# Kernel optimization log

Hardware: AMD Instinct MI355X
Metric: run time of the kernel (lower is better)

## Reference

```python
import jax, jax.numpy as jnp
import numpy as np

INIT_MEAN = 0.3


def _loo_sum(x, idx, n_seg):
    # leave-one-out segment sum along edge axis; x: [B, E]
    tot = jnp.zeros((x.shape[0], n_seg), x.dtype).at[:, idx].add(x)
    return tot[:, idx] - x


def _check_node_process(x, chk_idx, n_checks):
    # 2*atanh( prod_{e' in check, e'!=e} tanh(x_e'/2) ) via log-magnitude + sign
    t = jnp.tanh(0.5 * x)
    abs_t = jnp.clip(jnp.abs(t), 1e-12, None)
    log_loo = _loo_sum(jnp.log(abs_t), chk_idx, n_checks)
    neg = (t < 0).astype(x.dtype)
    neg_loo = _loo_sum(neg, chk_idx, n_checks)
    sign = 1.0 - 2.0 * jnp.mod(neg_loo, 2.0)
    prod = jnp.clip(sign * jnp.exp(log_loo), -1.0 + 1e-7, 1.0 - 1e-7)
    return 2.0 * jnp.arctanh(prod)


def setup_inputs() -> dict:
    N, M, DV, DC, ITERS, B = 8192, 4096, 3, 6, 5, 1024
    E = N * DV
    rng = np.random.RandomState(0)
    # regular (3,6) Tanner graph: each variable has 3 edges, each check 6
    var_idx = np.repeat(np.arange(N, dtype=np.int32), DV)
    chk_idx = rng.permutation(np.repeat(np.arange(M, dtype=np.int32), DC)).astype(np.int32)
    key = jax.random.key(0)
    k1, k2, k3 = jax.random.split(key, 3)
    llr = jax.random.normal(k1, (B, N), dtype=jnp.float32)
    vnode_w = INIT_MEAN + 0.02 * jax.random.normal(k2, (ITERS, E), dtype=jnp.float32)
    cnode_w = INIT_MEAN + 0.02 * jax.random.normal(k3, (ITERS, E), dtype=jnp.float32)
    return {
        "llr": llr,
        "vnode_w": vnode_w,
        "cnode_w": cnode_w,
        "var_idx": jnp.asarray(var_idx),
        "chk_idx": jnp.asarray(chk_idx),
        "n_checks": M,
    }


def reference(llr, vnode_w, cnode_w, var_idx, chk_idx, n_checks):
    B, N = llr.shape
    iters = vnode_w.shape[0]
    scattered_llr = llr[:, var_idx]            # [B, E]
    ext = jnp.zeros_like(scattered_llr)
    outs = []
    for i in range(iters):
        a_priori = _loo_sum(ext, var_idx, N) * vnode_w[i]
        ext = _check_node_process(a_priori + scattered_llr, chk_idx, n_checks) * cnode_w[i]
        out = jnp.zeros((B, N), llr.dtype).at[:, var_idx].add(ext) + llr
        outs.append(out)
    return jnp.stack(outs)  # [iters, B, N]
```

## Files before the change

kernel.cpp:

```cpp
#include <hip/hip_runtime.h>


#define N_VARS 8192
#define M_CHK  4096
#define ITERS  5
#define BATCH  1024
#define NEDGE  (N_VARS * 3)
#define TPB    1024
#define EPT    (NEDGE / TPB)
#define VPT    (N_VARS / TPB)
#define CPT    (M_CHK / TPB)
#define CSTRIDE 7

#define LOG2E_F 1.44269504f
#define LN2_F   0.69314718f
#define E_CLIP  0.99999988f

__device__ __forceinline__ float tanh_half(float x) {
    float a  = fabsf(x);
    float ee = __builtin_amdgcn_exp2f(-a * LOG2E_F);
    float tt = (1.0f - ee) * __builtin_amdgcn_rcpf(1.0f + ee);
    unsigned sg = __float_as_uint(x) & 0x80000000u;
    return __uint_as_float(__float_as_uint(tt) | sg);
}

__device__ __forceinline__ float atanh2(float p) {
    p = fminf(fmaxf(p, -E_CLIP), E_CLIP);
    return LN2_F * (__builtin_amdgcn_logf(1.0f + p)
                  - __builtin_amdgcn_logf(1.0f - p));
}

__global__ void setup_slots(const int* __restrict__ chk,
                            unsigned* __restrict__ tbl,
                            int* __restrict__ cnt) {
    int e = blockIdx.x * 256 + threadIdx.x;
    if (e < NEDGE) {
        int c = chk[e];
        int slot = atomicAdd(&cnt[c], 1);
        tbl[e] = (unsigned)(c * CSTRIDE + slot);
    }
}

__global__ void __launch_bounds__(TPB, 4)
nsp_kernel(const float* __restrict__ llr,
           const float* __restrict__ vw,
           const float* __restrict__ cw,
           const unsigned* __restrict__ tbl,
           float* __restrict__ out)
{
    __shared__ float lds_m[M_CHK * CSTRIDE];

    const int b  = blockIdx.x;
    const int t  = threadIdx.x;
    const int e0 = t * EPT;
    const int n0 = t * VPT;

    float llr_v[VPT];
    {
        const float4* p = (const float4*)(llr + (size_t)b * N_VARS + n0);
        float4 a = p[0], c = p[1];
        llr_v[0] = a.x; llr_v[1] = a.y; llr_v[2] = a.z; llr_v[3] = a.w;
        llr_v[4] = c.x; llr_v[5] = c.y; llr_v[6] = c.z; llr_v[7] = c.w;
    }

    unsigned pa[EPT / 2];
    {
        const uint4* p = (const uint4*)(tbl + e0);
#pragma unroll
        for (int k = 0; k < EPT / 4; ++k) {
            uint4 v = p[k];
            pa[2 * k]     = v.x | (v.y << 16);
            pa[2 * k + 1] = v.z | (v.w << 16);
        }
    }
#define ADDR(e) ((pa[(e) >> 1] >> (((e) & 1) * 16)) & 0xFFFFu)

    auto computeA4 = [&](int v0, const float* cwr, const float* vwr,
                         float* op, const float* rr) {
        float outb[4];
#pragma unroll
        for (int vv = 0; vv < 4; ++vv) {
            const int v = v0 + vv;
            float x0 = rr[3 * v + 0] * cwr[3 * v + 0];
            float x1 = rr[3 * v + 1] * cwr[3 * v + 1];
            float x2 = rr[3 * v + 2] * cwr[3 * v + 2];
            float s  = x0 + x1 + x2;
            outb[vv] = s + llr_v[v];
#pragma unroll
            for (int j = 0; j < 3; ++j) {
                const int e = 3 * v + j;
                float extj = (j == 0) ? x0 : (j == 1) ? x1 : x2;
                float x = (s - extj) * vwr[e] + llr_v[v];
                lds_m[ADDR(e)] = tanh_half(x);
            }
        }
        *((float4*)(op + v0)) = make_float4(outb[0], outb[1], outb[2], outb[3]);
    };

    for (int it = 0; it < ITERS; ++it) {
        if (it == 0) {
#pragma unroll
            for (int v = 0; v < VPT; ++v) {
                float p = tanh_half(llr_v[v]);
#pragma unroll
                for (int j = 0; j < 3; ++j)
                    lds_m[ADDR(3 * v + j)] = p;
            }
        } else {
            const float* cwr = cw + (size_t)(it - 1) * NEDGE + e0;
            const float* vwr = vw + (size_t)it * NEDGE + e0;
            float* op = out + ((size_t)(it - 1) * BATCH + b) * N_VARS + n0;
            float rr[EPT];
#pragma unroll
            for (int e = 0; e < EPT; ++e)
                rr[e] = lds_m[ADDR(e)];
            computeA4(0, cwr, vwr, op, rr);
            computeA4(4, cwr, vwr, op, rr);
        }
        __syncthreads();

        {
            float tv[CPT][6];
#pragma unroll
            for (int k = 0; k < CPT; ++k) {
                const int base = (t + k * TPB) * CSTRIDE;
#pragma unroll
                for (int i = 0; i < 6; ++i)
                    tv[k][i] = lds_m[base + i];
            }
#pragma unroll
            for (int k = 0; k < CPT; ++k) {
                const int base = (t + k * TPB) * CSTRIDE;
                float t0 = tv[k][0], t1 = tv[k][1], t2 = tv[k][2];
                float t3 = tv[k][3], t4 = tv[k][4], t5 = tv[k][5];
                float p1 = t0 * t1;
                float p2 = p1 * t2;
                float p3 = p2 * t3;
                float p4 = p3 * t4;
                float s4 = t5 * t4;
                float s3 = s4 * t3;
                float s2 = s3 * t2;
                float s1 = s2 * t1;
                lds_m[base + 0] = atanh2(s1);
                lds_m[base + 1] = atanh2(t0 * s2);
                lds_m[base + 2] = atanh2(p1 * s3);
                lds_m[base + 3] = atanh2(p2 * s4);
                lds_m[base + 4] = atanh2(p3 * t5);
                lds_m[base + 5] = atanh2(p4);
            }
        }
        __syncthreads();
    }

    {
        const float* cwr = cw + (size_t)(ITERS - 1) * NEDGE + e0;
        float* op = out + ((size_t)(ITERS - 1) * BATCH + b) * N_VARS + n0;
        float rr[EPT];
#pragma unroll
        for (int e = 0; e < EPT; ++e)
            rr[e] = lds_m[ADDR(e)];
        float outb[VPT];
#pragma unroll
        for (int v = 0; v < VPT; ++v) {
            outb[v] = rr[3 * v + 0] * cwr[3 * v + 0]
                    + rr[3 * v + 1] * cwr[3 * v + 1]
                    + rr[3 * v + 2] * cwr[3 * v + 2]
                    + llr_v[v];
        }
        ((float4*)op)[0] = make_float4(outb[0], outb[1], outb[2], outb[3]);
        ((float4*)op)[1] = make_float4(outb[4], outb[5], outb[6], outb[7]);
    }
#undef ADDR
}

extern "C" void kernel_launch(void* const* d_in, const int* in_sizes, int n_in,
                              void* d_out, int out_size, void* d_ws, size_t ws_size,
                              hipStream_t stream) {
    const float* llr = (const float*)d_in[0];
    const float* vw  = (const float*)d_in[1];
    const float* cw  = (const float*)d_in[2];
    const int*   chk = (const int*)d_in[4];
    float* out = (float*)d_out;

    unsigned* tbl = (unsigned*)d_ws;
    int*      cnt = (int*)((char*)d_ws + NEDGE * sizeof(unsigned));

    hipMemsetAsync(cnt, 0, M_CHK * sizeof(int), stream);
    setup_slots<<<(NEDGE + 255) / 256, 256, 0, stream>>>(chk, tbl, cnt);
    nsp_kernel<<<BATCH, TPB, 0, stream>>>(llr, vw, cw, tbl, out);
}
```

Measured before the change: 305.9 us.

## Assign check-node slots greedily to minimize LDS bank conflicts on edge writes

Replaces the atomic slot assignment with a two-step build: first collect each check's six edges, then a single-block kernel assigns slots within each check so that edges written by the same wavefront at the same unroll step land in different LDS banks. It keeps per-(wave, edge-position) bank counters in shared memory and picks the least-used free slot. The aim is fewer LDS bank conflicts in the scattered writes and reads of the main kernel. In exchange it adds a serial single-block setup kernel to every launch, and the heuristic runs without any synchronization between threads.

```diff
diff --git a/kernel.cpp b/kernel.cpp
--- a/kernel.cpp
+++ b/kernel.cpp
@@ -11,6 +11,7 @@
 #define VPT    (N_VARS / TPB)
 #define CPT    (M_CHK / TPB)
 #define CSTRIDE 7
+#define NGRP   (16 * 24)
 
 #define LOG2E_F 1.44269504f
 #define LN2_F   0.69314718f
@@ -30,14 +31,47 @@
                   - __builtin_amdgcn_logf(1.0f - p));
 }
 
-__global__ void setup_slots(const int* __restrict__ chk,
-                            unsigned* __restrict__ tbl,
-                            int* __restrict__ cnt) {
+__global__ void build_ce(const int* __restrict__ chk,
+                         int* __restrict__ ce,
+                         int* __restrict__ cnt) {
     int e = blockIdx.x * 256 + threadIdx.x;
     if (e < NEDGE) {
         int c = chk[e];
-        int slot = atomicAdd(&cnt[c], 1);
-        tbl[e] = (unsigned)(c * CSTRIDE + slot);
+        int r = atomicAdd(&cnt[c], 1);
+        ce[c * 6 + r] = e;
+    }
+}
+
+__global__ __launch_bounds__(1024)
+void assign_slots(const int* __restrict__ ce,
+                  unsigned* __restrict__ tbl) {
+    __shared__ unsigned gcnt[NGRP * 32];
+    const int tid = threadIdx.x;
+    for (int i = tid; i < NGRP * 32; i += 1024)
+        gcnt[i] = 0;
+    __syncthreads();
+#pragma unroll
+    for (int k = 0; k < M_CHK / 1024; ++k) {
+        const int c = tid + k * 1024;
+        const int cbase = c * CSTRIDE;
+        unsigned avail = 0x3Fu;
+        for (int r = 0; r < 6; ++r) {
+            int e = ce[c * 6 + r];
+            int t = e / 24;
+            int g = (t >> 6) * 24 + (e - t * 24);
+            int best = -1;
+            unsigned bestc = ~0u;
+#pragma unroll
+            for (int s = 0; s < 6; ++s) {
+                if ((avail >> s) & 1u) {
+                    unsigned cc = gcnt[g * 32 + ((cbase + s) & 31)];
+                    if (cc < bestc) { bestc = cc; best = s; }
+                }
+            }
+            atomicAdd(&gcnt[g * 32 + ((cbase + best) & 31)], 1u);
+            avail &= ~(1u << best);
+            tbl[e] = (unsigned)(cbase + best);
+        }
     }
 }
 
@@ -184,8 +218,11 @@
 
     unsigned* tbl = (unsigned*)d_ws;
     int*      cnt = (int*)((char*)d_ws + NEDGE * sizeof(unsigned));
+    int*      ce  = (int*)((char*)d_ws + NEDGE * sizeof(unsigned)
+                                       + M_CHK * sizeof(int));
 
     hipMemsetAsync(cnt, 0, M_CHK * sizeof(int), stream);
-    setup_slots<<<(NEDGE + 255) / 256, 256, 0, stream>>>(chk, tbl, cnt);
+    build_ce<<<(NEDGE + 255) / 256, 256, 0, stream>>>(chk, ce, cnt);
+    assign_slots<<<1, 1024, 0, stream>>>(ce, tbl);
     nsp_kernel<<<BATCH, TPB, 0, stream>>>(llr, vw, cw, tbl, out);
 }
```

After: 325.0 us. +6.3%, slower.
